# Kernel optimization log

Measured on AMD Instinct MI355X. Metric: run time of the kernel, lower is better.

Reference implementation:

```python
import jax, jax.numpy as jnp
import numpy as np

N = 100000      # nodes
E = 640000      # edges
IN = 100        # in_channels
OUT = 128       # out_channels
H, D = 4, 32    # heads, per-head dim (OUT = H*D)
MSG, TOUT, ETD, NET = 16, 100, 8, 4
EDGE_COLS = MSG + TOUT + 2        # 118 raw edge_attr columns
EDIM = (MSG - 1) + ETD + TOUT + 2 # 125 processed edge feature dim
SCALE = 1.0 / np.sqrt(D)


def _lin(k, fi, fo):
    return (jax.random.normal(k, (fi, fo), jnp.float32) / np.sqrt(fi)).astype(jnp.float32)


def setup_inputs() -> dict:
    key = jax.random.key(0)
    ks = jax.random.split(key, 24)
    x = jax.random.normal(ks[0], (N, IN), jnp.float32)
    edge_index = jax.random.randint(ks[1], (2, E), 0, N, dtype=jnp.int32)
    ea = jax.random.normal(ks[2], (E, EDGE_COLS), jnp.float32)
    etype = jax.random.randint(ks[3], (E,), 0, NET).astype(jnp.float32)
    edge_attr = ea.at[:, 3].set(etype)
    emb = jax.random.normal(ks[4], (NET, ETD), jnp.float32)
    inp = {"x": x, "edge_index": edge_index, "edge_attr": edge_attr, "emb": emb}
    # conv1: in=IN, conv2: in=OUT; lin_edge has no bias (PyG default)
    for i, fi in ((1, IN), (2, OUT)):
        base = 5 + (i - 1) * 8
        inp[f"w{i}q"] = _lin(ks[base + 0], fi, OUT)
        inp[f"b{i}q"] = jnp.zeros((OUT,), jnp.float32)
        inp[f"w{i}k"] = _lin(ks[base + 1], fi, OUT)
        inp[f"b{i}k"] = jnp.zeros((OUT,), jnp.float32)
        inp[f"w{i}v"] = _lin(ks[base + 2], fi, OUT)
        inp[f"b{i}v"] = jnp.zeros((OUT,), jnp.float32)
        inp[f"w{i}e"] = _lin(ks[base + 3], EDIM, OUT)
        inp[f"w{i}s"] = _lin(ks[base + 4], fi, OUT)
        inp[f"b{i}s"] = jnp.zeros((OUT,), jnp.float32)
    return inp


def _seg_softmax(logits, seg, n):
    # logits: [E, H], softmax over edges sharing the same target node
    m = jax.ops.segment_max(logits, seg, num_segments=n)      # [N, H]
    ex = jnp.exp(logits - m[seg])
    s = jax.ops.segment_sum(ex, seg, num_segments=n)          # [N, H]
    return ex / (s[seg] + 1e-16)


def _tconv(x, src, dst, e, wq, bq, wk, bk, wv, bv, we, ws, bs):
    n = x.shape[0]
    q = (x @ wq + bq)[dst].reshape(-1, H, D)   # gather targets
    k = (x @ wk + bk)[src].reshape(-1, H, D)   # gather sources
    v = (x @ wv + bv)[src].reshape(-1, H, D)
    ee = (e @ we).reshape(-1, H, D)            # per-edge projection
    alpha = jnp.sum(q * (k + ee), axis=-1) * SCALE          # [E, H]
    a = _seg_softmax(alpha, dst, n)                          # scatter-softmax
    msg = (v + ee) * a[..., None]                            # [E, H, D]
    out = jax.ops.segment_sum(msg, dst, num_segments=n).reshape(n, H * D)
    return out + x @ ws + bs                                 # root/skip connection


def reference(x, edge_index, edge_attr, emb,
              w1q, b1q, w1k, b1k, w1v, b1v, w1e, w1s, b1s,
              w2q, b2q, w2k, b2k, w2v, b2v, w2e, w2s, b2s):
    src, dst = edge_index[0], edge_index[1]
    cont = edge_attr[:, :3]
    etype = edge_attr[:, 3].astype(jnp.int32)
    rest = edge_attr[:, 4:]
    e = jnp.concatenate([cont, rest, emb[etype]], axis=-1)   # [E, EDIM]
    h = jax.nn.relu(_tconv(x, src, dst, e, w1q, b1q, w1k, b1k, w1v, b1v, w1e, w1s, b1s))
    return _tconv(h, src, dst, e, w2q, b2q, w2k, b2k, w2v, b2v, w2e, w2s, b2s)
```

## Files before the change

kernel.cpp:

```cpp
#include <hip/hip_runtime.h>

#define NN 100000
#define NE 640000
#define OUTF 128
#define K1 100
#define KE 118
#define KPAD 128
#define ASTR 136
#define ATT_SCALE 0.17677669529663687f
#define NSCANB 391
#define ETILES 5

typedef __attribute__((ext_vector_type(8))) short short8;
typedef __attribute__((ext_vector_type(4))) float f32x4;

__device__ __forceinline__ unsigned short f2bf(float f) {
    unsigned u = __float_as_uint(f);
    u += 0x7FFFu + ((u >> 16) & 1u);
    return (unsigned short)(u >> 16);
}
__device__ __forceinline__ float bf2f(unsigned short h) {
    return __uint_as_float(((unsigned)h) << 16);
}

__global__ void prep_weights(
    const float* __restrict__ w1q, const float* __restrict__ w1k,
    const float* __restrict__ w1v, const float* __restrict__ w1s,
    const float* __restrict__ w2q, const float* __restrict__ w2k,
    const float* __restrict__ w2v, const float* __restrict__ w2s,
    const float* __restrict__ we1, const float* __restrict__ we2,
    const float* __restrict__ emb,
    const float* __restrict__ b1q, const float* __restrict__ b1k,
    const float* __restrict__ b1v, const float* __restrict__ b1s,
    const float* __restrict__ b2q, const float* __restrict__ b2k,
    const float* __restrict__ b2v, const float* __restrict__ b2s,
    unsigned short* __restrict__ WT1, unsigned short* __restrict__ WT2,
    unsigned short* __restrict__ WmT1, unsigned short* __restrict__ WmT2,
    float* __restrict__ bias1, float* __restrict__ bias2)
{
    int idx = blockIdx.x * blockDim.x + threadIdx.x;
    int stride = gridDim.x * blockDim.x;
    for (int i = idx; i < 512 * KPAD; i += stride) {
        int col = i >> 7, k = i & 127;
        int which = col >> 7, c = col & 127;
        const float* s1 = (which == 0) ? w1q : (which == 1) ? w1k : (which == 2) ? w1v : w1s;
        const float* s2 = (which == 0) ? w2q : (which == 1) ? w2k : (which == 2) ? w2v : w2s;
        float v1 = (k < K1) ? s1[k * OUTF + c] : 0.f;
        float v2 = s2[k * OUTF + c];
        WT1[i] = f2bf(v1); WT2[i] = f2bf(v2);
    }
    for (int i = idx; i < OUTF * KPAD; i += stride) {
        int col = i >> 7, k = i & 127;
        float v1 = 0.f, v2 = 0.f;
        if (k < 3)                 { v1 = we1[k * OUTF + col];       v2 = we2[k * OUTF + col]; }
        else if (k >= 4 && k < KE) { v1 = we1[(k - 1) * OUTF + col]; v2 = we2[(k - 1) * OUTF + col]; }
        else if (k >= KE && k < KE + 4) {
            int t = k - KE;
            #pragma unroll
            for (int r = 0; r < 8; r++) {
                float ev = emb[t * 8 + r];
                v1 += ev * we1[(117 + r) * OUTF + col];
                v2 += ev * we2[(117 + r) * OUTF + col];
            }
        }
        WmT1[i] = f2bf(v1); WmT2[i] = f2bf(v2);
    }
    for (int i = idx; i < 512; i += stride) {
        int which = i >> 7, c = i & 127;
        const float* sb1 = (which == 0) ? b1q : (which == 1) ? b1k : (which == 2) ? b1v : b1s;
        const float* sb2 = (which == 0) ? b2q : (which == 1) ? b2k : (which == 2) ? b2v : b2s;
        bias1[i] = sb1[c]; bias2[i] = sb2[c];
    }
}

__global__ void hist_kernel(const int* __restrict__ dstI, int* __restrict__ cnt) {
    int e = blockIdx.x * 256 + threadIdx.x;
    if (e < NE) atomicAdd(&cnt[dstI[e]], 1);
}
__global__ void scan1(const int* __restrict__ cnt, int* __restrict__ S1, int* __restrict__ bsum) {
    __shared__ int sd[256];
    int t = blockIdx.x * 256 + threadIdx.x;
    sd[threadIdx.x] = (t < NN) ? cnt[t] : 0;
    __syncthreads();
    for (int off = 1; off < 256; off <<= 1) {
        int x = (threadIdx.x >= off) ? sd[threadIdx.x - off] : 0;
        __syncthreads();
        sd[threadIdx.x] += x;
        __syncthreads();
    }
    if (t < NN) S1[t] = sd[threadIdx.x];
    if (threadIdx.x == 255) bsum[blockIdx.x] = sd[255];
}
__global__ void scan2(const int* __restrict__ bsum, int* __restrict__ boff) {
    __shared__ int sd[512];
    int t = threadIdx.x;
    sd[t] = (t < NSCANB) ? bsum[t] : 0;
    __syncthreads();
    for (int off = 1; off < 512; off <<= 1) {
        int x = (t >= off) ? sd[t - off] : 0;
        __syncthreads();
        sd[t] += x;
        __syncthreads();
    }
    if (t < NSCANB) boff[t] = (t == 0) ? 0 : sd[t - 1];
}
__global__ void scan3(const int* __restrict__ S1, const int* __restrict__ boff,
                      const int* __restrict__ cnt,
                      int* __restrict__ row_start, int* __restrict__ cursor) {
    int t = blockIdx.x * 256 + threadIdx.x;
    if (t < NN) {
        int incl = S1[t] + boff[t >> 8];
        row_start[t + 1] = incl;
        cursor[t] = incl - cnt[t];
        if (t == 0) row_start[0] = 0;
    }
}
__global__ void scatter_csr(const int* __restrict__ srcI, const int* __restrict__ dstI,
                            int* __restrict__ cursor,
                            int* __restrict__ csr_src, int* __restrict__ csr_eid) {
    int e = blockIdx.x * 256 + threadIdx.x;
    if (e < NE) {
        int j = atomicAdd(&cursor[dstI[e]], 1);
        csr_src[j] = srcI[e];
        csr_eid[j] = e;
    }
}

__global__ __launch_bounds__(256) void node_mfma(
    const float* __restrict__ X, int ldx, int Kdim, int relu, int n,
    const unsigned short* __restrict__ WT, const float* __restrict__ bias,
    float* __restrict__ Qp, unsigned short* __restrict__ KVp, float* __restrict__ Hp)
{
    __shared__ unsigned short Alds[128][ASTR];
    int tid = threadIdx.x;
    int rowbase = (blockIdx.x >> 2) * 128;
    int nb = blockIdx.x & 3;

    for (int idx = tid; idx < 128 * 68; idx += 256) {
        int r = idx / 68, kv = idx % 68;
        int k = kv * 2;
        float2 v = make_float2(0.f, 0.f);
        int gr = rowbase + r;
        if (gr < n && k < Kdim) v = *(const float2*)(X + (size_t)gr * ldx + k);
        if (relu) { v.x = fmaxf(v.x, 0.f); v.y = fmaxf(v.y, 0.f); }
        unsigned pv = (unsigned)f2bf(v.x) | ((unsigned)f2bf(v.y) << 16);
        *(unsigned*)&Alds[r][k] = pv;
    }
    __syncthreads();

    int lane = tid & 63, wid = tid >> 6;
    int wm = wid >> 1, wn = wid & 1;
    int l15 = lane & 15, l4 = lane >> 4;

    f32x4 acc[4][4];
    #pragma unroll
    for (int mf = 0; mf < 4; mf++)
        #pragma unroll
        for (int nf = 0; nf < 4; nf++)
            acc[mf][nf] = (f32x4){0.f, 0.f, 0.f, 0.f};

    const unsigned short* wbase = WT + (size_t)(nb * 128 + wn * 64 + l15) * KPAD + l4 * 8;
    #pragma unroll
    for (int ks = 0; ks < 4; ks++) {
        short8 af[4], bfr[4];
        #pragma unroll
        for (int mf = 0; mf < 4; mf++)
            af[mf] = *(const short8*)&Alds[wm * 64 + mf * 16 + l15][ks * 32 + l4 * 8];
        #pragma unroll
        for (int nf = 0; nf < 4; nf++)
            bfr[nf] = *(const short8*)(wbase + (size_t)nf * 16 * KPAD + ks * 32);
        #pragma unroll
        for (int mf = 0; mf < 4; mf++)
            #pragma unroll
            for (int nf = 0; nf < 4; nf++)
                acc[mf][nf] = __builtin_amdgcn_mfma_f32_16x16x32_bf16(af[mf], bfr[nf], acc[mf][nf], 0, 0, 0);
    }
    __syncthreads();

    if (nb == 1 || nb == 2) {
        #pragma unroll
        for (int nf = 0; nf < 4; nf++) {
            int col = wn * 64 + nf * 16 + l15;
            float bv = bias[nb * 128 + col];
            #pragma unroll
            for (int mf = 0; mf < 4; mf++)
                #pragma unroll
                for (int rr = 0; rr < 4; rr++)
                    Alds[wm * 64 + mf * 16 + l4 * 4 + rr][col] = f2bf(acc[mf][nf][rr] + bv);
        }
        __syncthreads();
        int off = (nb == 1) ? 0 : 128;
        #pragma unroll
        for (int it = 0; it < 8; it++) {
            int idx = it * 256 + tid;
            int row = idx >> 4, c8 = (idx & 15) * 8;
            if (rowbase + row < n) {
                uint4 v = *(const uint4*)&Alds[row][c8];
                *(uint4*)(KVp + (size_t)(rowbase + row) * 256 + off + c8) = v;
            }
        }
    } else {
        float* Yp = (nb == 0) ? Qp : Hp;
        float scale = (nb == 0) ? ATT_SCALE : 1.f;
        float (*Sf)[68] = (float (*)[68])Alds;
        #pragma unroll
        for (int h = 0; h < 2; h++) {
            if (wn == h) {
                #pragma unroll
                for (int nf = 0; nf < 4; nf++) {
                    int col = wn * 64 + nf * 16 + l15;
                    float bv = bias[nb * 128 + col];
                    #pragma unroll
                    for (int mf = 0; mf < 4; mf++)
                        #pragma unroll
                        for (int rr = 0; rr < 4; rr++)
                            Sf[wm * 64 + mf * 16 + l4 * 4 + rr][nf * 16 + l15] =
                                (acc[mf][nf][rr] + bv) * scale;
                }
            }
            __syncthreads();
            #pragma unroll
            for (int it = 0; it < 8; it++) {
                int idx = it * 256 + tid;
                int row = idx >> 4, c4 = (idx & 15) * 4;
                if (rowbase + row < n) {
                    float4 v = *(const float4*)&Sf[row][c4];
                    *(float4*)(Yp + (size_t)(rowbase + row) * OUTF + h * 64 + c4) = v;
                }
            }
            if (h == 0) __syncthreads();
        }
    }
}

__global__ __launch_bounds__(256) void edge_mfma_fused(
    const float* __restrict__ EA,
    const unsigned short* __restrict__ WmT1, const unsigned short* __restrict__ WmT2,
    unsigned short* __restrict__ EE1, unsigned short* __restrict__ EE2)
{
    __shared__ unsigned short Tlds[64][ASTR];
    int tid = threadIdx.x;
    int lane = tid & 63, w = tid >> 6;
    int l15 = lane & 15, l4 = lane >> 4;
    int rbase = w * 16;
    int tile0 = blockIdx.x * ETILES;

    auto load_tile = [&](int tile, short8* af) {
        const float* rp = EA + (size_t)(tile * 64 + rbase + l15) * KE;
        float etf = rp[3];
        #pragma unroll
        for (int ks = 0; ks < 4; ks++) {
            int cbase = ks * 32 + l4 * 8;
            float2 t0 = make_float2(0.f, 0.f), t1 = t0, t2 = t0, t3 = t0;
            if (cbase + 2 <= KE) t0 = *(const float2*)(rp + cbase);
            if (cbase + 4 <= KE) t1 = *(const float2*)(rp + cbase + 2);
            if (cbase + 6 <= KE) t2 = *(const float2*)(rp + cbase + 4);
            if (cbase + 8 <= KE) t3 = *(const float2*)(rp + cbase + 6);
            float fv[8] = {t0.x, t0.y, t1.x, t1.y, t2.x, t2.y, t3.x, t3.y};
            #pragma unroll
            for (int j = 0; j < 8; j++) {
                int col = cbase + j;
                float v = (col == 3) ? 0.f : fv[j];
                af[ks][j] = f2bf(v);
            }
        }
        int oh = KE + (int)etf;
        #pragma unroll
        for (int j = 0; j < 8; j++) {
            int col = 96 + l4 * 8 + j;
            if (col == oh) af[3][j] = 0x3F80;
        }
    };
    auto do_layer = [&](const unsigned short* __restrict__ WmT, unsigned short* __restrict__ EEc,
                        int e0, const short8* af) {
        f32x4 acc[8];
        #pragma unroll
        for (int nf = 0; nf < 8; nf++) acc[nf] = (f32x4){0.f, 0.f, 0.f, 0.f};

        #pragma unroll
        for (int ks = 0; ks < 4; ks++) {
            short8 bfr[8];
            #pragma unroll
            for (int nf = 0; nf < 8; nf++)
                bfr[nf] = *(const short8*)(WmT + (size_t)(nf * 16 + l15) * KPAD + ks * 32 + l4 * 8);
            #pragma unroll
            for (int nf = 0; nf < 8; nf++)
                acc[nf] = __builtin_amdgcn_mfma_f32_16x16x32_bf16(af[ks], bfr[nf], acc[nf], 0, 0, 0);
        }
        #pragma unroll
        for (int nf = 0; nf < 8; nf++)
            #pragma unroll
            for (int rr = 0; rr < 4; rr++)
                Tlds[rbase + l4 * 4 + rr][nf * 16 + l15] = f2bf(acc[nf][rr]);
        #pragma unroll
        for (int it = 0; it < 4; it++) {
            int t2 = it * 64 + lane;
            int rid = t2 >> 4, c8 = (t2 & 15) * 8;
            uint4 v = *(const uint4*)&Tlds[rbase + rid][c8];
            *(uint4*)(EEc + ((size_t)(e0 + rbase + rid)) * 128 + c8) = v;
        }
    };

    short8 afA[4];
    load_tile(tile0, afA);

    #pragma unroll
    for (int t = 0; t < ETILES; t++) {
        int e0 = (tile0 + t) * 64;
        do_layer(WmT1, EE1, e0, afA);
        short8 afB[4];
        if (t + 1 < ETILES) load_tile(tile0 + t + 1, afB);
        do_layer(WmT2, EE2, e0, afA);
        if (t + 1 < ETILES) {
            afA[0] = afB[0]; afA[1] = afB[1]; afA[2] = afB[2]; afA[3] = afB[3];
        }
    }
}

__global__ __launch_bounds__(256) void attn_node(
    const float* __restrict__ Qp, const unsigned short* __restrict__ KVp,
    const unsigned short* __restrict__ EEc,
    const int* __restrict__ row_start, const int* __restrict__ csr_src,
    const int* __restrict__ csr_eid,
    const float* __restrict__ Hskip, float* __restrict__ Out)
{
    int lane = threadIdx.x & 63;
    int gw = (int)((blockIdx.x * (size_t)blockDim.x + threadIdx.x) >> 6);
    int nW = (gridDim.x * blockDim.x) >> 6;
    int c2 = lane * 2;

    for (int d = gw; d < NN; d += nW) {
        int rs = row_start[d], re = row_start[d + 1];
        float2 q = *(const float2*)(Qp + (size_t)d * OUTF + c2);
        float m = -3.4e38f, s = 0.f, a0 = 0.f, a1 = 0.f;

        int j0 = (rs < re) ? rs : 0;
        int jlast = (rs < re) ? re - 1 : 0;
        int j1 = (j0 + 1 <= jlast) ? j0 + 1 : jlast;
        int j2 = (j0 + 2 <= jlast) ? j0 + 2 : jlast;
        int sjA = csr_src[j0], ejA = csr_eid[j0];
        int sjB = csr_src[j1], ejB = csr_eid[j1];
        int sjC = csr_src[j2], ejC = csr_eid[j2];
        unsigned kA = *(const unsigned*)(KVp + (size_t)sjA * 256 + c2);
        unsigned vA = *(const unsigned*)(KVp + (size_t)sjA * 256 + 128 + c2);
        unsigned eA = *(const unsigned*)(EEc + (size_t)ejA * 128 + c2);
        unsigned kB = *(const unsigned*)(KVp + (size_t)sjB * 256 + c2);
        unsigned vB = *(const unsigned*)(KVp + (size_t)sjB * 256 + 128 + c2);
        unsigned eB = *(const unsigned*)(EEc + (size_t)ejB * 128 + c2);

        for (int j = rs; j < re; j++) {
            unsigned kC = *(const unsigned*)(KVp + (size_t)sjC * 256 + c2);
            unsigned vC = *(const unsigned*)(KVp + (size_t)sjC * 256 + 128 + c2);
            unsigned eC = *(const unsigned*)(EEc + (size_t)ejC * 128 + c2);
            int j3 = (j + 3 <= jlast) ? j + 3 : jlast;
            int sjD = csr_src[j3], ejD = csr_eid[j3];

            float e0 = bf2f((unsigned short)(eA & 0xFFFFu));
            float e1 = bf2f((unsigned short)(eA >> 16));
            float k0 = bf2f((unsigned short)(kA & 0xFFFFu));
            float k1 = bf2f((unsigned short)(kA >> 16));
            float v0 = bf2f((unsigned short)(vA & 0xFFFFu));
            float v1 = bf2f((unsigned short)(vA >> 16));

            float t = q.x * (k0 + e0) + q.y * (k1 + e1);
            t += __shfl_xor(t, 1); t += __shfl_xor(t, 2);
            t += __shfl_xor(t, 4); t += __shfl_xor(t, 8);
            float alpha = t;
            float mn = fmaxf(m, alpha);
            float r = __expf(m - mn);
            float p = __expf(alpha - mn);
            s = s * r + p;
            a0 = a0 * r + p * (v0 + e0);
            a1 = a1 * r + p * (v1 + e1);
            m = mn;
            kA = kB; vA = vB; eA = eB;
            kB = kC; vB = vC; eB = eC;
            sjC = sjD; ejC = ejD;
        }
        float inv = 1.f / (s + 1e-16f);
        float2 h = *(const float2*)(Hskip + (size_t)d * OUTF + c2);
        float2 o;
        o.x = a0 * inv + h.x;
        o.y = a1 * inv + h.y;
        *(float2*)(Out + (size_t)d * OUTF + c2) = o;
    }
}

extern "C" void kernel_launch(void* const* d_in, const int* in_sizes, int n_in,
                              void* d_out, int out_size, void* d_ws, size_t ws_size,
                              hipStream_t stream) {
    const float* x    = (const float*)d_in[0];
    const int*   ei   = (const int*)d_in[1];
    const float* ea   = (const float*)d_in[2];
    const float* emb  = (const float*)d_in[3];
    const float* w1q  = (const float*)d_in[4];  const float* b1q = (const float*)d_in[5];
    const float* w1k  = (const float*)d_in[6];  const float* b1k = (const float*)d_in[7];
    const float* w1v  = (const float*)d_in[8];  const float* b1v = (const float*)d_in[9];
    const float* w1e  = (const float*)d_in[10];
    const float* w1s  = (const float*)d_in[11]; const float* b1s = (const float*)d_in[12];
    const float* w2q  = (const float*)d_in[13]; const float* b2q = (const float*)d_in[14];
    const float* w2k  = (const float*)d_in[15]; const float* b2k = (const float*)d_in[16];
    const float* w2v  = (const float*)d_in[17]; const float* b2v = (const float*)d_in[18];
    const float* w2e  = (const float*)d_in[19];
    const float* w2s  = (const float*)d_in[20]; const float* b2s = (const float*)d_in[21];

    const int* srcI = ei;
    const int* dstI = ei + NE;

    float* Q = (float*)d_ws;
    unsigned short* KV = (unsigned short*)(Q + (size_t)NN * OUTF);
    float* H = (float*)(KV + (size_t)NN * 256);
    unsigned short* EE1 = (unsigned short*)(H + (size_t)NN * OUTF);
    unsigned short* EE2 = EE1 + (size_t)NE * 128;
    int* csr_src   = (int*)(EE2 + (size_t)NE * 128);
    int* csr_eid   = csr_src + NE;
    int* row_start = csr_eid + NE;
    int* cursor    = row_start + NN + 1;
    int* cnt       = cursor + NN;
    int* S1        = cnt + NN;
    int* bsum      = S1 + NN;
    int* boff      = bsum + NSCANB;
    unsigned short* WT1  = (unsigned short*)(boff + NSCANB + 1);
    unsigned short* WT2  = WT1 + 512 * KPAD;
    unsigned short* WmT1 = WT2 + 512 * KPAD;
    unsigned short* WmT2 = WmT1 + OUTF * KPAD;
    float* bias1 = (float*)(WmT2 + OUTF * KPAD);
    float* bias2 = bias1 + 512;

    prep_weights<<<128, 256, 0, stream>>>(w1q, w1k, w1v, w1s, w2q, w2k, w2v, w2s,
                                          w1e, w2e, emb,
                                          b1q, b1k, b1v, b1s, b2q, b2k, b2v, b2s,
                                          WT1, WT2, WmT1, WmT2, bias1, bias2);
    hipMemsetAsync(cnt, 0, (size_t)NN * sizeof(int), stream);
    hist_kernel<<<NE / 256, 256, 0, stream>>>(dstI, cnt);
    scan1<<<NSCANB, 256, 0, stream>>>(cnt, S1, bsum);
    scan2<<<1, 512, 0, stream>>>(bsum, boff);
    scan3<<<NSCANB, 256, 0, stream>>>(S1, boff, cnt, row_start, cursor);
    scatter_csr<<<NE / 256, 256, 0, stream>>>(srcI, dstI, cursor, csr_src, csr_eid);

    int ngrid = ((NN + 127) / 128) * 4;
    int egrid = NE / (64 * ETILES);

    node_mfma<<<ngrid, 256, 0, stream>>>(x, K1, K1, 0, NN, WT1, bias1, Q, KV, H);
    edge_mfma_fused<<<egrid, 256, 0, stream>>>(ea, WmT1, WmT2, EE1, EE2);
    attn_node<<<4096, 256, 0, stream>>>(Q, KV, EE1, row_start, csr_src, csr_eid, H, H);

    node_mfma<<<ngrid, 256, 0, stream>>>(H, OUTF, OUTF, 1, NN, WT2, bias2, Q, KV, (float*)d_out);
    attn_node<<<4096, 256, 0, stream>>>(Q, KV, EE2, row_start, csr_src, csr_eid, (float*)d_out, (float*)d_out);
}
```

Measured before the change: 986.5 us.

## Stream edge-attribute tiles into double-buffered LDS via async global-to-LDS loads

The edge projection kernel no longer loads edge-attribute rows from global memory into registers. Each wave now issues direct global-to-LDS 16-byte loads of its 16 raw rows into one of two per-wave LDS stage buffers. The next tile is prefetched while the current one is converted and multiplied, with hand-coded vmcnt waits that account for outstanding stores. The same stage buffer is reused as the transpose scratch for writing results. This aims to hide global latency and give coalesced loads, but it raises LDS use to about 60KB per block, which may lower occupancy, and it depends on exact vmcnt accounting.

```diff
diff --git a/kernel.cpp b/kernel.cpp
--- a/kernel.cpp
+++ b/kernel.cpp
@@ -10,6 +10,9 @@
 #define ATT_SCALE 0.17677669529663687f
 #define NSCANB 391
 #define ETILES 5
+#define ROWB 472
+#define WCHUNK 7552
+#define STAGEB (4 * WCHUNK)
 
 typedef __attribute__((ext_vector_type(8))) short short8;
 typedef __attribute__((ext_vector_type(4))) float f32x4;
@@ -21,6 +24,11 @@
 }
 __device__ __forceinline__ float bf2f(unsigned short h) {
     return __uint_as_float(((unsigned)h) << 16);
+}
+__device__ __forceinline__ void gld_lds16(const void* g, void* l) {
+    __builtin_amdgcn_global_load_lds(
+        (const __attribute__((address_space(1))) unsigned int*)g,
+        (__attribute__((address_space(3))) unsigned int*)l, 16, 0, 0);
 }
 
 __global__ void prep_weights(
@@ -238,24 +246,35 @@
     const unsigned short* __restrict__ WmT1, const unsigned short* __restrict__ WmT2,
     unsigned short* __restrict__ EE1, unsigned short* __restrict__ EE2)
 {
-    __shared__ unsigned short Tlds[64][ASTR];
+    __shared__ char stage[2][STAGEB];
     int tid = threadIdx.x;
     int lane = tid & 63, w = tid >> 6;
     int l15 = lane & 15, l4 = lane >> 4;
-    int rbase = w * 16;
     int tile0 = blockIdx.x * ETILES;
 
-    auto load_tile = [&](int tile, short8* af) {
-        const float* rp = EA + (size_t)(tile * 64 + rbase + l15) * KE;
-        float etf = rp[3];
+    char* wb0 = stage[0] + w * WCHUNK;
+    char* wb1 = stage[1] + w * WCHUNK;
+    const char* gEA = (const char*)EA;
+
+    auto issue_stage = [&](int tile, char* ldst) {
+        const char* gsrc = gEA + (size_t)(tile * 64 + w * 16) * ROWB + lane * 16;
+        #pragma unroll
+        for (int i = 0; i < 7; i++)
+            gld_lds16(gsrc + i * 1024, ldst + i * 1024);
+        if (lane < 24)
+            gld_lds16(gsrc + 7 * 1024, ldst + 7 * 1024);
+    };
+    auto read_frag = [&](const char* wb, short8* af) {
+        const float* rowp = (const float*)(wb + l15 * ROWB);
+        float etf = rowp[3];
         #pragma unroll
         for (int ks = 0; ks < 4; ks++) {
             int cbase = ks * 32 + l4 * 8;
             float2 t0 = make_float2(0.f, 0.f), t1 = t0, t2 = t0, t3 = t0;
-            if (cbase + 2 <= KE) t0 = *(const float2*)(rp + cbase);
-            if (cbase + 4 <= KE) t1 = *(const float2*)(rp + cbase + 2);
-            if (cbase + 6 <= KE) t2 = *(const float2*)(rp + cbase + 4);
-            if (cbase + 8 <= KE) t3 = *(const float2*)(rp + cbase + 6);
+            if (cbase + 2 <= KE) t0 = *(const float2*)(rowp + cbase);
+            if (cbase + 4 <= KE) t1 = *(const float2*)(rowp + cbase + 2);
+            if (cbase + 6 <= KE) t2 = *(const float2*)(rowp + cbase + 4);
+            if (cbase + 8 <= KE) t3 = *(const float2*)(rowp + cbase + 6);
             float fv[8] = {t0.x, t0.y, t1.x, t1.y, t2.x, t2.y, t3.x, t3.y};
             #pragma unroll
             for (int j = 0; j < 8; j++) {
@@ -272,7 +291,7 @@
         }
     };
     auto do_layer = [&](const unsigned short* __restrict__ WmT, unsigned short* __restrict__ EEc,
-                        int e0, const short8* af) {
+                        int e0, const short8* af, char* wb) {
         f32x4 acc[8];
         #pragma unroll
         for (int nf = 0; nf < 8; nf++) acc[nf] = (f32x4){0.f, 0.f, 0.f, 0.f};
@@ -287,33 +306,35 @@
             for (int nf = 0; nf < 8; nf++)
                 acc[nf] = __builtin_amdgcn_mfma_f32_16x16x32_bf16(af[ks], bfr[nf], acc[nf], 0, 0, 0);
         }
+        unsigned short* tb = (unsigned short*)wb;
         #pragma unroll
         for (int nf = 0; nf < 8; nf++)
             #pragma unroll
             for (int rr = 0; rr < 4; rr++)
-                Tlds[rbase + l4 * 4 + rr][nf * 16 + l15] = f2bf(acc[nf][rr]);
+                tb[(l4 * 4 + rr) * 136 + nf * 16 + l15] = f2bf(acc[nf][rr]);
         #pragma unroll
         for (int it = 0; it < 4; it++) {
             int t2 = it * 64 + lane;
             int rid = t2 >> 4, c8 = (t2 & 15) * 8;
-            uint4 v = *(const uint4*)&Tlds[rbase + rid][c8];
-            *(uint4*)(EEc + ((size_t)(e0 + rbase + rid)) * 128 + c8) = v;
+            uint4 v = *(const uint4*)(tb + rid * 136 + c8);
+            *(uint4*)(EEc + ((size_t)(e0 + w * 16 + rid)) * 128 + c8) = v;
         }
     };
 
+    issue_stage(tile0, wb0);
+
     short8 afA[4];
-    load_tile(tile0, afA);
-
     #pragma unroll
     for (int t = 0; t < ETILES; t++) {
+        char* cur = (t & 1) ? wb1 : wb0;
+        char* nxt = (t & 1) ? wb0 : wb1;
+        if (t + 1 < ETILES) issue_stage(tile0 + t + 1, nxt);
+        if (t == 0 || t == ETILES - 1) asm volatile("s_waitcnt vmcnt(8)" ::: "memory");
+        else                           asm volatile("s_waitcnt vmcnt(16)" ::: "memory");
+        read_frag(cur, afA);
         int e0 = (tile0 + t) * 64;
-        do_layer(WmT1, EE1, e0, afA);
-        short8 afB[4];
-        if (t + 1 < ETILES) load_tile(tile0 + t + 1, afB);
-        do_layer(WmT2, EE2, e0, afA);
-        if (t + 1 < ETILES) {
-            afA[0] = afB[0]; afA[1] = afB[1]; afA[2] = afB[2]; afA[3] = afB[3];
-        }
+        do_layer(WmT1, EE1, e0, afA, cur);
+        do_layer(WmT2, EE2, e0, afA, cur);
     }
 }
 
```

Result: slower. 1.045 ms (+6.0%).
